# Kernel tuning notes

Hardware: AMD Instinct MI355X
Metric: run time of the kernel (lower is better)

Reference implementation:

```python
import jax, jax.numpy as jnp
import numpy as np

DIM = 1024
NUM_HEADS = 16
HEAD_DIM = DIM // NUM_HEADS  # 64; only used for the softmax scale


def setup_inputs() -> dict:
    key = jax.random.key(0)
    ks = jax.random.split(key, 9)
    s = 1.0 / np.sqrt(DIM)
    return {
        "x": jax.random.normal(ks[0], (2, 4096, DIM), dtype=jnp.float32),
        "Wq": jax.random.normal(ks[1], (DIM, DIM), dtype=jnp.float32) * s,
        "bq": jnp.zeros((DIM,), dtype=jnp.float32),
        "Wk": jax.random.normal(ks[2], (DIM, DIM), dtype=jnp.float32) * s,
        "bk": jnp.zeros((DIM,), dtype=jnp.float32),
        "Wv": jax.random.normal(ks[3], (DIM, DIM), dtype=jnp.float32) * s,
        "bv": jnp.zeros((DIM,), dtype=jnp.float32),
        "Wo": jax.random.normal(ks[4], (DIM, DIM), dtype=jnp.float32) * s,
        "bo": jnp.zeros((DIM,), dtype=jnp.float32),
    }


def reference(x, Wq, bq, Wk, bk, Wv, bv, Wo, bo):
    # Projections (nn.Linear equivalents)
    q = jnp.einsum("bsd,df->bsf", x, Wq) + bq
    k = jnp.einsum("bsd,df->bsf", x, Wk) + bk
    v = jnp.einsum("bsd,df->bsf", x, Wv) + bv
    # Full-dim attention (no head split); scale uses head_dim per original code.
    scale = 1.0 / np.sqrt(HEAD_DIM)
    scores = jnp.einsum("bqd,bkd->bqk", q, k) * scale  # [B, S, S]
    attn = jax.nn.softmax(scores, axis=-1)
    out = jnp.einsum("bqk,bkd->bqd", attn, v)
    return jnp.einsum("bsd,df->bsf", out, Wo) + bo
```

## Files before the change

### kernel.cpp

```cpp
#include <hip/hip_runtime.h>

typedef unsigned short u16;
using bf16x8  = __attribute__((ext_vector_type(8))) __bf16;
using floatx4 = __attribute__((ext_vector_type(4))) float;

__device__ __forceinline__ u16 f2bf(float f) {
  unsigned int u = __builtin_bit_cast(unsigned int, f);
  u += 0x7fffu + ((u >> 16) & 1u);
  return (u16)(u >> 16);
}
__device__ __forceinline__ float bf2f(u16 h) {
  unsigned int u = ((unsigned int)h) << 16;
  return __builtin_bit_cast(float, u);
}

#define AS1(p) ((const __attribute__((address_space(1))) void*)(p))
#define AS3(p) ((__attribute__((address_space(3))) void*)(p))

#define NE_PROLOGUE(bmv, bnv)                                                \
  __shared__ u16 lds[65536];                                    \
  const int tid = threadIdx.x;                                               \
  const int w = tid >> 6, lane = tid & 63;                                   \
  const int wm = (w >> 2) * 128, wn = (w & 3) * 64;                          \
  const int wm16 = (w >> 2) * 8;           \
  const int wn4  = (w & 3) * 4;            \
  const long bm = (bmv), bn = (bnv);                                         \
  floatx4 acc[8][4] = {};                                                    \
  const int fr = lane & 15;                                                  \
  const int kq = (lane >> 4) * 8;                                            \
  const int oc = (lane >> 4) * 4;                                            \
         \
  const int swz  = (lane * 16) ^ (((lane >> 5) & 1) << 5);                   \
  const int srow = swz >> 6;                  \
  const int scol = (swz & 63) >> 1;           \
  const int st0  = w * 2;                      \
                        \
  const int aoff = fr * 64 + ((kq * 2) ^ (((fr >> 3) & 1) << 5));

#define NE_SETUP_PTRS(Abp, Bbp, ldK)                                         \
  const u16* A0p = (Abp) + (long)(st0 * 16 + srow) * (ldK) + scol;           \
  const u16* A1p = A0p + 16L * (ldK);                                        \
  const u16* B0p = (Bbp) + (long)(st0 * 16 + srow) * (ldK) + scol;           \
  const u16* B1p = B0p + 16L * (ldK);

#define NE_SA(T)                                                             \
  { u16* d_ = lds + (((T) & 3) * 16384) + st0 * 512;                         \
    long o_ = (long)(T) * 32;                                                \
    __builtin_amdgcn_global_load_lds(AS1(A0p + o_), AS3(d_), 16, 0, 0);      \
    __builtin_amdgcn_global_load_lds(AS1(A1p + o_), AS3(d_ + 512), 16, 0, 0); }
#define NE_SB(T)                                                             \
  { u16* d_ = lds + (((T) & 3) * 16384) + 8192 + st0 * 512;                  \
    long o_ = (long)(T) * 32;                                                \
    __builtin_amdgcn_global_load_lds(AS1(B0p + o_), AS3(d_), 16, 0, 0);      \
    __builtin_amdgcn_global_load_lds(AS1(B1p + o_), AS3(d_ + 512), 16, 0, 0); }

#define NE_TILE_G(T, NT, MF)                                                 \
  {                                                                          \
    const char* sb_ = (const char*)lds + ((T) & 3) * 32768;                  \
    if ((T) + 2 < (NT)) NE_SB((T) + 2)                                       \
    if ((T) + 3 < (NT)) NE_SA((T) + 3)                                       \
    bf16x8 af[4], bf[4];                                                     \
    _Pragma("unroll")                                                        \
    for (int i = 0; i < 4; ++i)                                              \
      af[i] = *(const bf16x8*)(sb_ + (wm16 + i) * 1024 + aoff);              \
    _Pragma("unroll")                                                        \
    for (int i = 0; i < 4; ++i)                                              \
      bf[i] = *(const bf16x8*)(sb_ + 16384 + (wn4 + i) * 1024 + aoff);       \
    asm volatile("s_waitcnt lgkmcnt(0)" ::: "memory");                       \
    __builtin_amdgcn_sched_barrier(0);                                       \
    __builtin_amdgcn_s_setprio(1);                                           \
    _Pragma("unroll")                                                        \
    for (int mi = 0; mi < 4; ++mi)                                           \
      _Pragma("unroll")                                                      \
      for (int ni = 0; ni < 4; ++ni)                                         \
        acc[mi][ni] = MF(mi, ni, acc[mi][ni]);                               \
    __builtin_amdgcn_s_setprio(0);                                           \
    _Pragma("unroll")                                                        \
    for (int i = 0; i < 4; ++i)                                              \
      af[i] = *(const bf16x8*)(sb_ + (wm16 + 4 + i) * 1024 + aoff);          \
    asm volatile("s_waitcnt lgkmcnt(0)" ::: "memory");                       \
    __builtin_amdgcn_sched_barrier(0);                                       \
    __builtin_amdgcn_s_setprio(1);                                           \
    _Pragma("unroll")                                                        \
    for (int mi = 0; mi < 4; ++mi)                                           \
      _Pragma("unroll")                                                      \
      for (int ni = 0; ni < 4; ++ni)                                         \
        acc[4 + mi][ni] = MF(mi, ni, acc[4 + mi][ni]);                       \
    __builtin_amdgcn_s_setprio(0);                                           \
    if ((T) < (NT) - 3)       { asm volatile("s_waitcnt vmcnt(6)" ::: "memory"); } \
    else if ((T) == (NT) - 3) { asm volatile("s_waitcnt vmcnt(4)" ::: "memory"); } \
    else if ((T) == (NT) - 2) { asm volatile("s_waitcnt vmcnt(0)" ::: "memory"); } \
    __builtin_amdgcn_s_barrier();                                            \
    __builtin_amdgcn_sched_barrier(0);                                       \
  }

#define NE_MF_SWAP(mi, ni, c) __builtin_amdgcn_mfma_f32_16x16x32_bf16(bf[ni], af[mi], (c), 0, 0, 0)
#define NE_MF_NS(mi, ni, c)   __builtin_amdgcn_mfma_f32_16x16x32_bf16(af[mi], bf[ni], (c), 0, 0, 0)
#define NE_TILE(T, NT)    NE_TILE_G(T, NT, NE_MF_SWAP)
#define NE_TILE_NS(T, NT) NE_TILE_G(T, NT, NE_MF_NS)

#define NE_START()                                                           \
  NE_SA(0) NE_SB(0) NE_SA(1) NE_SB(1) NE_SA(2)                               \
  asm volatile("s_waitcnt vmcnt(6)" ::: "memory");                           \
  __builtin_amdgcn_s_barrier();                                              \
  __builtin_amdgcn_sched_barrier(0);

#define NE2_PROLOGUE(bmv, bnv)                                               \
  __shared__ u16 lds[49152];                                     \
  const int tid = threadIdx.x;                                               \
  const int w = tid >> 6, lane = tid & 63;                                   \
  const int wm = (w >> 2) * 64, wn = (w & 3) * 64;                           \
  const int wm4 = (w >> 2) * 4;            \
  const int wn4 = (w & 3) * 4;             \
  const long bm = (bmv), bn = (bnv);                                         \
  floatx4 acc[4][4] = {};                                                    \
  const int fr = lane & 15;                                                  \
  const int kq = (lane >> 4) * 8;                                            \
  const int oc = (lane >> 4) * 4;                                            \
  const int swz  = (lane * 16) ^ (((lane >> 5) & 1) << 5);                   \
  const int srow = swz >> 6;                                                 \
  const int scol = (swz & 63) >> 1;                                          \
  const int st0  = w * 2;                                                    \
  const int aoff = fr * 64 + ((kq * 2) ^ (((fr >> 3) & 1) << 5));

#define NE2_SETUP_PTRS(Abp, Bbp, ldK)                                        \
  const u16* A0p = (Abp) + (long)(w * 16 + srow) * (ldK) + scol;             \
  const u16* B0p = (Bbp) + (long)(st0 * 16 + srow) * (ldK) + scol;           \
  const u16* B1p = B0p + 16L * (ldK);

#define NE2_SA(T)                                                            \
  { u16* d_ = lds + (((T) & 3) * 12288) + w * 512;                           \
    __builtin_amdgcn_global_load_lds(AS1(A0p + (long)(T) * 32), AS3(d_), 16, 0, 0); }
#define NE2_SB(T)                                                            \
  { u16* d_ = lds + (((T) & 3) * 12288) + 4096 + st0 * 512;                  \
    long o_ = (long)(T) * 32;                                                \
    __builtin_amdgcn_global_load_lds(AS1(B0p + o_), AS3(d_), 16, 0, 0);      \
    __builtin_amdgcn_global_load_lds(AS1(B1p + o_), AS3(d_ + 512), 16, 0, 0); }

#define NE2_TILE_G(T, NT, MF)                                                \
  {                                                                          \
    const char* sb_ = (const char*)lds + ((T) & 3) * 24576;                  \
    if ((T) + 2 < (NT)) NE2_SB((T) + 2)                                      \
    if ((T) + 3 < (NT)) NE2_SA((T) + 3)                                      \
    bf16x8 af[4], bf[4];                                                     \
    _Pragma("unroll")                                                        \
    for (int i = 0; i < 4; ++i)                                              \
      af[i] = *(const bf16x8*)(sb_ + (wm4 + i) * 1024 + aoff);               \
    _Pragma("unroll")                                                        \
    for (int i = 0; i < 4; ++i)                                              \
      bf[i] = *(const bf16x8*)(sb_ + 8192 + (wn4 + i) * 1024 + aoff);        \
    asm volatile("s_waitcnt lgkmcnt(0)" ::: "memory");                       \
    __builtin_amdgcn_sched_barrier(0);                                       \
    __builtin_amdgcn_s_setprio(1);                                           \
    _Pragma("unroll")                                                        \
    for (int mi = 0; mi < 4; ++mi)                                           \
      _Pragma("unroll")                                                      \
      for (int ni = 0; ni < 4; ++ni)                                         \
        acc[mi][ni] = MF(mi, ni, acc[mi][ni]);                               \
    __builtin_amdgcn_s_setprio(0);                                           \
    if ((T) < (NT) - 3)       { asm volatile("s_waitcnt vmcnt(4)" ::: "memory"); } \
    else if ((T) == (NT) - 3) { asm volatile("s_waitcnt vmcnt(3)" ::: "memory"); } \
    else if ((T) == (NT) - 2) { asm volatile("s_waitcnt vmcnt(0)" ::: "memory"); } \
    __builtin_amdgcn_s_barrier();                                            \
    __builtin_amdgcn_sched_barrier(0);                                       \
  }

#define NE2_TILE(T, NT)    NE2_TILE_G(T, NT, NE_MF_SWAP)
#define NE2_TILE_NS(T, NT) NE2_TILE_G(T, NT, NE_MF_NS)

#define NE2_START()                                                          \
  NE2_SA(0) NE2_SB(0) NE2_SA(1) NE2_SB(1) NE2_SA(2)                          \
  asm volatile("s_waitcnt vmcnt(4)" ::: "memory");                           \
  __builtin_amdgcn_s_barrier();                                              \
  __builtin_amdgcn_sched_barrier(0);

__global__ __launch_bounds__(512, 2) void gemm_qk_exp(
    const u16* __restrict__ q, const u16* __restrict__ k,
    u16* __restrict__ probs, float* __restrict__ lpartT, float alpha)
{
  const int N = 4096;
  const int xcd = blockIdx.x;
  const int j = blockIdx.y;
  const long b = xcd >> 2;
  const int by = (xcd & 3) * 4 + (j & 3);
  const int bx = j >> 2;

  NE_PROLOGUE((long)by * 256, (long)bx * 256);
  const u16* Ab = q + b * 4096 * 1024 + bm * 1024;
  const u16* Bb = k + b * 4096 * 1024 + bn * 1024;
  NE_SETUP_PTRS(Ab, Bb, 1024);
  u16* P = probs + b * 4096L * 4096;
  float* lp = lpartT + b * 4096 * 64;

  NE_START()
  for (int T = 0; T < 32; ++T) NE_TILE(T, 32)

  const float a2 = alpha * 1.44269504f;
  const int cg = bx * 4 + (w & 3);
#pragma unroll
  for (int mi = 0; mi < 8; ++mi) {
    long row = bm + wm + mi * 16 + fr;
    float rs = 0.f;
#pragma unroll
    for (int ni = 0; ni < 4; ++ni) {
      long colb = bn + wn + ni * 16 + oc;
      float e0 = __builtin_amdgcn_exp2f(acc[mi][ni][0] * a2);
      float e1 = __builtin_amdgcn_exp2f(acc[mi][ni][1] * a2);
      float e2 = __builtin_amdgcn_exp2f(acc[mi][ni][2] * a2);
      float e3 = __builtin_amdgcn_exp2f(acc[mi][ni][3] * a2);
      rs += (e0 + e1) + (e2 + e3);
      ushort4 o;
      o.x = f2bf(e0); o.y = f2bf(e1); o.z = f2bf(e2); o.w = f2bf(e3);
      *(ushort4*)(P + row * N + colb) = o;
    }
    rs += __shfl_xor(rs, 16);
    rs += __shfl_xor(rs, 32);
    if (lane < 16)
      lp[(bm + wm + mi * 16 + lane) * 64 + cg] = rs;
  }
}

__global__ __launch_bounds__(512, 2) void gemm_pv_splitk2(
    const u16* __restrict__ probs, const u16* __restrict__ vT,
    u16* __restrict__ pA, u16* __restrict__ pB)
{
  const int xcd = blockIdx.x;
  const int j = blockIdx.y;
  const long b = xcd >> 2;
  const int sp = (xcd >> 1) & 1;
  const int by = (xcd & 1) * 8 + (j & 7);
  const int bx = j >> 3;

  NE_PROLOGUE((long)by * 256, (long)bx * 256);
  const u16* Ab = probs + b * 4096L * 4096 + bm * 4096 + sp * 2048;
  const u16* Bb = vT + b * 1024L * 4096 + bn * 4096 + sp * 2048;
  NE_SETUP_PTRS(Ab, Bb, 4096);
  u16* part = (b ? pB : pA) + (long)sp * 4096 * 1024;

  NE_START()
  for (int T = 0; T < 64; ++T) NE_TILE(T, 64)

#pragma unroll
  for (int mi = 0; mi < 8; ++mi) {
    long row = bm + wm + mi * 16 + fr;
#pragma unroll
    for (int ni = 0; ni < 4; ++ni) {
      long colb = bn + wn + ni * 16 + oc;
      ushort4 o;
      o.x = f2bf(acc[mi][ni][0]);
      o.y = f2bf(acc[mi][ni][1]);
      o.z = f2bf(acc[mi][ni][2]);
      o.w = f2bf(acc[mi][ni][3]);
      *(ushort4*)(part + row * 1024 + colb) = o;
    }
  }
}

__global__ __launch_bounds__(512, 2) void gemm_qkv(
    const u16* __restrict__ A, const u16* __restrict__ Bt,
    u16* __restrict__ qb, u16* __restrict__ kb, u16* __restrict__ vT,
    const float* __restrict__ bq, const float* __restrict__ bk,
    const float* __restrict__ bv)
{
  const int xcd = blockIdx.x;
  const int j = blockIdx.y;
  const int by = xcd * 8 + (j & 7);
  const int bx = j >> 3;

  NE2_PROLOGUE((long)by * 128, (long)bx * 256);
  const u16* Ab = A + bm * 1024;
  const u16* Bb = Bt + bn * 1024;
  NE2_SETUP_PTRS(Ab, Bb, 1024);

  if (bn < 2048) {
    NE2_START()
    for (int T = 0; T < 32; ++T) NE2_TILE(T, 32)
    u16* C = (bn < 1024) ? qb : kb;
    const float* bias = (bn < 1024) ? bq : bk;
#pragma unroll
    for (int mi = 0; mi < 4; ++mi) {
      long row = bm + wm + mi * 16 + fr;
#pragma unroll
      for (int ni = 0; ni < 4; ++ni) {
        long colg = bn + wn + ni * 16 + oc;
        long cc = colg & 1023;
        float4 bv4 = *(const float4*)(bias + cc);
        ushort4 o;
        o.x = f2bf(acc[mi][ni][0] + bv4.x);
        o.y = f2bf(acc[mi][ni][1] + bv4.y);
        o.z = f2bf(acc[mi][ni][2] + bv4.z);
        o.w = f2bf(acc[mi][ni][3] + bv4.w);
        *(ushort4*)(C + row * 1024 + cc) = o;
      }
    }
  } else {
    NE2_START()
    for (int T = 0; T < 32; ++T) NE2_TILE_NS(T, 32)
    const int orow = (lane >> 4) * 4;
    const long b_ = bm >> 12;
    const long s0 = (bm & 4095) + wm;
    u16* vb = vT + b_ * (1024L * 4096);
#pragma unroll
    for (int ni = 0; ni < 4; ++ni) {
      long d = bn + wn + ni * 16 + fr - 2048;
      float bvv = bv[d];
#pragma unroll
      for (int mi = 0; mi < 4; ++mi) {
        long s = s0 + mi * 16 + orow;
        ushort4 o;
        o.x = f2bf(acc[mi][ni][0] + bvv);
        o.y = f2bf(acc[mi][ni][1] + bvv);
        o.z = f2bf(acc[mi][ni][2] + bvv);
        o.w = f2bf(acc[mi][ni][3] + bvv);
        *(ushort4*)(vb + d * 4096L + s) = o;
      }
    }
  }
}

__global__ __launch_bounds__(512, 2) void gemm_bt(
    const u16* __restrict__ A, const u16* __restrict__ Bt,
    float* __restrict__ Cout, const float* __restrict__ bias)
{
  const int xcd = blockIdx.x;
  const int j = blockIdx.y;
  const int by = xcd * 8 + (j & 7);
  const int bx = j >> 3;

  NE2_PROLOGUE((long)by * 128, (long)bx * 256);
  const u16* Ab = A + bm * 1024;
  const u16* Bb = Bt + bn * 1024;
  NE2_SETUP_PTRS(Ab, Bb, 1024);

  NE2_START()
  for (int T = 0; T < 32; ++T) NE2_TILE(T, 32)

#pragma unroll
  for (int mi = 0; mi < 4; ++mi) {
    long row = bm + wm + mi * 16 + fr;
#pragma unroll
    for (int ni = 0; ni < 4; ++ni) {
      long colb = bn + wn + ni * 16 + oc;
      float4 bv4 = *(const float4*)(bias + colb);
      float4 o;
      o.x = acc[mi][ni][0] + bv4.x;
      o.y = acc[mi][ni][1] + bv4.y;
      o.z = acc[mi][ni][2] + bv4.z;
      o.w = acc[mi][ni][3] + bv4.w;
      *(float4*)(Cout + row * 1024 + colb) = o;
    }
  }
}

__global__ __launch_bounds__(256) void reduce2_div_row(
    const u16* __restrict__ pA, const u16* __restrict__ pB,
    const float* __restrict__ lpartT, u16* __restrict__ ob)
{
  const int row = blockIdx.x;
  const long b = blockIdx.y;
  const int tid = threadIdx.x;
  const u16* part = b ? pB : pA;
  const float* lp = lpartT + b * 4096 * 64;
  __shared__ float sl;
  if (tid < 64) {
    float s = lp[(long)row * 64 + tid];
#pragma unroll
    for (int off = 32; off; off >>= 1) s += __shfl_down(s, off);
    if (tid == 0) sl = s;
  }
  __syncthreads();
  const float inv = 1.0f / sl;
  const long base = (long)row * 1024 + tid * 4;
  float acc4[4] = {0.f, 0.f, 0.f, 0.f};
#pragma unroll
  for (int s = 0; s < 2; ++s) {
    ushort4 p = *(const ushort4*)(part + (long)s * 4096 * 1024 + base);
    acc4[0] += bf2f(p.x); acc4[1] += bf2f(p.y);
    acc4[2] += bf2f(p.z); acc4[3] += bf2f(p.w);
  }
  ushort4 o;
  o.x = f2bf(acc4[0] * inv);
  o.y = f2bf(acc4[1] * inv);
  o.z = f2bf(acc4[2] * inv);
  o.w = f2bf(acc4[3] * inv);
  *(ushort4*)(ob + b * 4096L * 1024 + base) = o;
}

__global__ __launch_bounds__(256) void prep(
    const float* __restrict__ x, u16* __restrict__ xb,
    const float* __restrict__ W0, const float* __restrict__ W1,
    const float* __restrict__ W2, const float* __restrict__ W3,
    u16* __restrict__ O0, u16* __restrict__ O1,
    u16* __restrict__ O2, u16* __restrict__ O3)
{
  __shared__ float tile[32][33];
  int blk = blockIdx.x;
  if (blk < 8192) {
    int i = blk * 256 + threadIdx.x;
    float4 f = ((const float4*)x)[i];
    ushort4 o;
    o.x = f2bf(f.x); o.y = f2bf(f.y); o.z = f2bf(f.z); o.w = f2bf(f.w);
    ((ushort4*)xb)[i] = o;
  } else {
    blk -= 8192;
    const int z = blk >> 10, t = blk & 1023;
    const float* in = (z == 0) ? W0 : (z == 1) ? W1 : (z == 2) ? W2 : W3;
    u16* outp = (z == 0) ? O0 : (z == 1) ? O1 : (z == 2) ? O2 : O3;
    const int bx = (t & 31) * 32, by = (t >> 5) * 32;
    const int tx = threadIdx.x & 31, ty = threadIdx.x >> 5;
    for (int i = ty; i < 32; i += 8)
      tile[i][tx] = in[(long)(by + i) * 1024 + bx + tx];
    __syncthreads();
    for (int i = ty; i < 32; i += 8)
      outp[(long)(bx + i) * 1024 + by + tx] = f2bf(tile[tx][i]);
  }
}

extern "C" void kernel_launch(void* const* d_in, const int* in_sizes, int n_in,
                              void* d_out, int out_size, void* d_ws, size_t ws_size,
                              hipStream_t stream) {
  const float* x  = (const float*)d_in[0];
  const float* Wq = (const float*)d_in[1];
  const float* bq = (const float*)d_in[2];
  const float* Wk = (const float*)d_in[3];
  const float* bk = (const float*)d_in[4];
  const float* Wv = (const float*)d_in[5];
  const float* bv = (const float*)d_in[6];
  const float* Wo = (const float*)d_in[7];
  const float* bo = (const float*)d_in[8];
  float* out = (float*)d_out;

  const int B = 2, S = 4096, D = 1024;
  const long MB = 1L << 20;

  char* w = (char*)d_ws;
  u16* qb  = (u16*)(w);
  u16* kb  = (u16*)(w + 16 * MB);
  u16* vT  = (u16*)(w + 32 * MB);
  u16* xb  = (u16*)(w + 48 * MB);
  u16* ob  = xb;
  u16* WqkvT = (u16*)(w + 64 * MB);
  u16* WoT = WqkvT + 3072L * 1024;
  u16* probs = (u16*)(w + 72 * MB);
  u16* partA = (u16*)(w);
  u16* partB = (u16*)(w + 136 * MB);
  float* lpartT = (float*)d_out;

  prep<<<dim3(8192 + 4096), 256, 0, stream>>>(
      x, xb, Wq, Wk, Wv, Wo,
      WqkvT, WqkvT + 1024L * 1024, WqkvT + 2048L * 1024, WoT);

  gemm_qkv<<<dim3(8, 96), 512, 0, stream>>>(
      xb, WqkvT, qb, kb, vT, bq, bk, bv);

  const float scale = 0.125f;
  gemm_qk_exp<<<dim3(8, 64), 512, 0, stream>>>(
      qb, kb, probs, lpartT, scale);
  gemm_pv_splitk2<<<dim3(8, 32), 512, 0, stream>>>(
      probs, vT, partA, partB);
  reduce2_div_row<<<dim3(S, B), 256, 0, stream>>>(partA, partB, lpartT, ob);

  gemm_bt<<<dim3(8, 32), 512, 0, stream>>>(ob, WoT, out, bo);
}
```

Before: 372.6 us.

## Switch attention GEMMs to 128x256 tiles with 3-stage LDS ring for higher occupancy

Drops the 256x256-tile NE pipeline and moves the QK^T-exp and PV split-K kernels onto the smaller 128x256 NE2 tile, doubling their grid sizes. The NE2 pipeline goes from a 4-slot to a 3-slot LDS ring, with A and B for tile T+2 prefetched together, which cuts shared memory per block. Launch bounds are raised from 2 to 4 blocks per CU to use the lower register and LDS footprint. This trades per-block data reuse and prefetch depth for more resident waves to hide latency.

```diff
diff --git a/kernel.cpp b/kernel.cpp
--- a/kernel.cpp
+++ b/kernel.cpp
@@ -17,96 +17,8 @@
 #define AS1(p) ((const __attribute__((address_space(1))) void*)(p))
 #define AS3(p) ((__attribute__((address_space(3))) void*)(p))
 
-#define NE_PROLOGUE(bmv, bnv)                                                \
-  __shared__ u16 lds[65536];                                    \
-  const int tid = threadIdx.x;                                               \
-  const int w = tid >> 6, lane = tid & 63;                                   \
-  const int wm = (w >> 2) * 128, wn = (w & 3) * 64;                          \
-  const int wm16 = (w >> 2) * 8;           \
-  const int wn4  = (w & 3) * 4;            \
-  const long bm = (bmv), bn = (bnv);                                         \
-  floatx4 acc[8][4] = {};                                                    \
-  const int fr = lane & 15;                                                  \
-  const int kq = (lane >> 4) * 8;                                            \
-  const int oc = (lane >> 4) * 4;                                            \
-         \
-  const int swz  = (lane * 16) ^ (((lane >> 5) & 1) << 5);                   \
-  const int srow = swz >> 6;                  \
-  const int scol = (swz & 63) >> 1;           \
-  const int st0  = w * 2;                      \
-                        \
-  const int aoff = fr * 64 + ((kq * 2) ^ (((fr >> 3) & 1) << 5));
-
-#define NE_SETUP_PTRS(Abp, Bbp, ldK)                                         \
-  const u16* A0p = (Abp) + (long)(st0 * 16 + srow) * (ldK) + scol;           \
-  const u16* A1p = A0p + 16L * (ldK);                                        \
-  const u16* B0p = (Bbp) + (long)(st0 * 16 + srow) * (ldK) + scol;           \
-  const u16* B1p = B0p + 16L * (ldK);
-
-#define NE_SA(T)                                                             \
-  { u16* d_ = lds + (((T) & 3) * 16384) + st0 * 512;                         \
-    long o_ = (long)(T) * 32;                                                \
-    __builtin_amdgcn_global_load_lds(AS1(A0p + o_), AS3(d_), 16, 0, 0);      \
-    __builtin_amdgcn_global_load_lds(AS1(A1p + o_), AS3(d_ + 512), 16, 0, 0); }
-#define NE_SB(T)                                                             \
-  { u16* d_ = lds + (((T) & 3) * 16384) + 8192 + st0 * 512;                  \
-    long o_ = (long)(T) * 32;                                                \
-    __builtin_amdgcn_global_load_lds(AS1(B0p + o_), AS3(d_), 16, 0, 0);      \
-    __builtin_amdgcn_global_load_lds(AS1(B1p + o_), AS3(d_ + 512), 16, 0, 0); }
-
-#define NE_TILE_G(T, NT, MF)                                                 \
-  {                                                                          \
-    const char* sb_ = (const char*)lds + ((T) & 3) * 32768;                  \
-    if ((T) + 2 < (NT)) NE_SB((T) + 2)                                       \
-    if ((T) + 3 < (NT)) NE_SA((T) + 3)                                       \
-    bf16x8 af[4], bf[4];                                                     \
-    _Pragma("unroll")                                                        \
-    for (int i = 0; i < 4; ++i)                                              \
-      af[i] = *(const bf16x8*)(sb_ + (wm16 + i) * 1024 + aoff);              \
-    _Pragma("unroll")                                                        \
-    for (int i = 0; i < 4; ++i)                                              \
-      bf[i] = *(const bf16x8*)(sb_ + 16384 + (wn4 + i) * 1024 + aoff);       \
-    asm volatile("s_waitcnt lgkmcnt(0)" ::: "memory");                       \
-    __builtin_amdgcn_sched_barrier(0);                                       \
-    __builtin_amdgcn_s_setprio(1);                                           \
-    _Pragma("unroll")                                                        \
-    for (int mi = 0; mi < 4; ++mi)                                           \
-      _Pragma("unroll")                                                      \
-      for (int ni = 0; ni < 4; ++ni)                                         \
-        acc[mi][ni] = MF(mi, ni, acc[mi][ni]);                               \
-    __builtin_amdgcn_s_setprio(0);                                           \
-    _Pragma("unroll")                                                        \
-    for (int i = 0; i < 4; ++i)                                              \
-      af[i] = *(const bf16x8*)(sb_ + (wm16 + 4 + i) * 1024 + aoff);          \
-    asm volatile("s_waitcnt lgkmcnt(0)" ::: "memory");                       \
-    __builtin_amdgcn_sched_barrier(0);                                       \
-    __builtin_amdgcn_s_setprio(1);                                           \
-    _Pragma("unroll")                                                        \
-    for (int mi = 0; mi < 4; ++mi)                                           \
-      _Pragma("unroll")                                                      \
-      for (int ni = 0; ni < 4; ++ni)                                         \
-        acc[4 + mi][ni] = MF(mi, ni, acc[4 + mi][ni]);                       \
-    __builtin_amdgcn_s_setprio(0);                                           \
-    if ((T) < (NT) - 3)       { asm volatile("s_waitcnt vmcnt(6)" ::: "memory"); } \
-    else if ((T) == (NT) - 3) { asm volatile("s_waitcnt vmcnt(4)" ::: "memory"); } \
-    else if ((T) == (NT) - 2) { asm volatile("s_waitcnt vmcnt(0)" ::: "memory"); } \
-    __builtin_amdgcn_s_barrier();                                            \
-    __builtin_amdgcn_sched_barrier(0);                                       \
-  }
-
-#define NE_MF_SWAP(mi, ni, c) __builtin_amdgcn_mfma_f32_16x16x32_bf16(bf[ni], af[mi], (c), 0, 0, 0)
-#define NE_MF_NS(mi, ni, c)   __builtin_amdgcn_mfma_f32_16x16x32_bf16(af[mi], bf[ni], (c), 0, 0, 0)
-#define NE_TILE(T, NT)    NE_TILE_G(T, NT, NE_MF_SWAP)
-#define NE_TILE_NS(T, NT) NE_TILE_G(T, NT, NE_MF_NS)
-
-#define NE_START()                                                           \
-  NE_SA(0) NE_SB(0) NE_SA(1) NE_SB(1) NE_SA(2)                               \
-  asm volatile("s_waitcnt vmcnt(6)" ::: "memory");                           \
-  __builtin_amdgcn_s_barrier();                                              \
-  __builtin_amdgcn_sched_barrier(0);
-
 #define NE2_PROLOGUE(bmv, bnv)                                               \
-  __shared__ u16 lds[49152];                                     \
+  __shared__ u16 lds[36864];                          \
   const int tid = threadIdx.x;                                               \
   const int w = tid >> 6, lane = tid & 63;                                   \
   const int wm = (w >> 2) * 64, wn = (w & 3) * 64;                           \
@@ -128,20 +40,22 @@
   const u16* B0p = (Bbp) + (long)(st0 * 16 + srow) * (ldK) + scol;           \
   const u16* B1p = B0p + 16L * (ldK);
 
-#define NE2_SA(T)                                                            \
-  { u16* d_ = lds + (((T) & 3) * 12288) + w * 512;                           \
-    __builtin_amdgcn_global_load_lds(AS1(A0p + (long)(T) * 32), AS3(d_), 16, 0, 0); }
-#define NE2_SB(T)                                                            \
-  { u16* d_ = lds + (((T) & 3) * 12288) + 4096 + st0 * 512;                  \
-    long o_ = (long)(T) * 32;                                                \
+#define NE2_SA(TT, S)                                                        \
+  { u16* d_ = lds + (S) * 12288 + w * 512;                                   \
+    __builtin_amdgcn_global_load_lds(AS1(A0p + (long)(TT) * 32), AS3(d_), 16, 0, 0); }
+#define NE2_SB(TT, S)                                                        \
+  { u16* d_ = lds + (S) * 12288 + 4096 + st0 * 512;                          \
+    long o_ = (long)(TT) * 32;                                               \
     __builtin_amdgcn_global_load_lds(AS1(B0p + o_), AS3(d_), 16, 0, 0);      \
     __builtin_amdgcn_global_load_lds(AS1(B1p + o_), AS3(d_ + 512), 16, 0, 0); }
 
-#define NE2_TILE_G(T, NT, MF)                                                \
+#define NE_MF_SWAP(mi, ni, c) __builtin_amdgcn_mfma_f32_16x16x32_bf16(bf[ni], af[mi], (c), 0, 0, 0)
+#define NE_MF_NS(mi, ni, c)   __builtin_amdgcn_mfma_f32_16x16x32_bf16(af[mi], bf[ni], (c), 0, 0, 0)
+
+#define NE2_TILE_G(T, NT, sR, sW, MF)                                        \
   {                                                                          \
-    const char* sb_ = (const char*)lds + ((T) & 3) * 24576;                  \
-    if ((T) + 2 < (NT)) NE2_SB((T) + 2)                                      \
-    if ((T) + 3 < (NT)) NE2_SA((T) + 3)                                      \
+    const char* sb_ = (const char*)lds + (sR) * 24576;                       \
+    if ((T) + 2 < (NT)) { NE2_SB((T) + 2, sW) NE2_SA((T) + 2, sW) }          \
     bf16x8 af[4], bf[4];                                                     \
     _Pragma("unroll")                                                        \
     for (int i = 0; i < 4; ++i)                                              \
@@ -158,23 +72,32 @@
       for (int ni = 0; ni < 4; ++ni)                                         \
         acc[mi][ni] = MF(mi, ni, acc[mi][ni]);                               \
     __builtin_amdgcn_s_setprio(0);                                           \
-    if ((T) < (NT) - 3)       { asm volatile("s_waitcnt vmcnt(4)" ::: "memory"); } \
-    else if ((T) == (NT) - 3) { asm volatile("s_waitcnt vmcnt(3)" ::: "memory"); } \
+    if ((T) < (NT) - 2)       { asm volatile("s_waitcnt vmcnt(3)" ::: "memory"); } \
     else if ((T) == (NT) - 2) { asm volatile("s_waitcnt vmcnt(0)" ::: "memory"); } \
     __builtin_amdgcn_s_barrier();                                            \
     __builtin_amdgcn_sched_barrier(0);                                       \
   }
 
-#define NE2_TILE(T, NT)    NE2_TILE_G(T, NT, NE_MF_SWAP)
-#define NE2_TILE_NS(T, NT) NE2_TILE_G(T, NT, NE_MF_NS)
-
 #define NE2_START()                                                          \
-  NE2_SA(0) NE2_SB(0) NE2_SA(1) NE2_SB(1) NE2_SA(2)                          \
-  asm volatile("s_waitcnt vmcnt(4)" ::: "memory");                           \
+  NE2_SA(0, 0) NE2_SB(0, 0) NE2_SA(1, 1) NE2_SB(1, 1)                        \
+  asm volatile("s_waitcnt vmcnt(3)" ::: "memory");                           \
   __builtin_amdgcn_s_barrier();                                              \
   __builtin_amdgcn_sched_barrier(0);
 
-__global__ __launch_bounds__(512, 2) void gemm_qk_exp(
+#define NE2_LOOP(NT, TILE_MACRO)                                             \
+  {                                                                          \
+    int sR = 0, sW = 2;                                                      \
+    for (int T = 0; T < (NT); ++T) {                                         \
+      TILE_MACRO(T, (NT), sR, sW)                                            \
+      sR = (sR == 2) ? 0 : sR + 1;                                           \
+      sW = (sW == 2) ? 0 : sW + 1;                                           \
+    }                                                                        \
+  }
+
+#define NE2_TILE(T, NT, sR, sW)    NE2_TILE_G(T, NT, sR, sW, NE_MF_SWAP)
+#define NE2_TILE_NS(T, NT, sR, sW) NE2_TILE_G(T, NT, sR, sW, NE_MF_NS)
+
+__global__ __launch_bounds__(512, 4) void gemm_qk_exp(
     const u16* __restrict__ q, const u16* __restrict__ k,
     u16* __restrict__ probs, float* __restrict__ lpartT, float alpha)
 {
@@ -182,23 +105,23 @@
   const int xcd = blockIdx.x;
   const int j = blockIdx.y;
   const long b = xcd >> 2;
-  const int by = (xcd & 3) * 4 + (j & 3);
-  const int bx = j >> 2;
-
-  NE_PROLOGUE((long)by * 256, (long)bx * 256);
+  const int by = (xcd & 3) * 8 + (j & 7);
+  const int bx = j >> 3;
+
+  NE2_PROLOGUE((long)by * 128, (long)bx * 256);
   const u16* Ab = q + b * 4096 * 1024 + bm * 1024;
   const u16* Bb = k + b * 4096 * 1024 + bn * 1024;
-  NE_SETUP_PTRS(Ab, Bb, 1024);
+  NE2_SETUP_PTRS(Ab, Bb, 1024);
   u16* P = probs + b * 4096L * 4096;
   float* lp = lpartT + b * 4096 * 64;
 
-  NE_START()
-  for (int T = 0; T < 32; ++T) NE_TILE(T, 32)
+  NE2_START()
+  NE2_LOOP(32, NE2_TILE)
 
   const float a2 = alpha * 1.44269504f;
   const int cg = bx * 4 + (w & 3);
 #pragma unroll
-  for (int mi = 0; mi < 8; ++mi) {
+  for (int mi = 0; mi < 4; ++mi) {
     long row = bm + wm + mi * 16 + fr;
     float rs = 0.f;
 #pragma unroll
@@ -220,7 +143,7 @@
   }
 }
 
-__global__ __launch_bounds__(512, 2) void gemm_pv_splitk2(
+__global__ __launch_bounds__(512, 4) void gemm_pv_splitk2(
     const u16* __restrict__ probs, const u16* __restrict__ vT,
     u16* __restrict__ pA, u16* __restrict__ pB)
 {
@@ -228,20 +151,20 @@
   const int j = blockIdx.y;
   const long b = xcd >> 2;
   const int sp = (xcd >> 1) & 1;
-  const int by = (xcd & 1) * 8 + (j & 7);
-  const int bx = j >> 3;
-
-  NE_PROLOGUE((long)by * 256, (long)bx * 256);
+  const int by = (xcd & 1) * 16 + (j & 15);
+  const int bx = j >> 4;
+
+  NE2_PROLOGUE((long)by * 128, (long)bx * 256);
   const u16* Ab = probs + b * 4096L * 4096 + bm * 4096 + sp * 2048;
   const u16* Bb = vT + b * 1024L * 4096 + bn * 4096 + sp * 2048;
-  NE_SETUP_PTRS(Ab, Bb, 4096);
+  NE2_SETUP_PTRS(Ab, Bb, 4096);
   u16* part = (b ? pB : pA) + (long)sp * 4096 * 1024;
 
-  NE_START()
-  for (int T = 0; T < 64; ++T) NE_TILE(T, 64)
-
-#pragma unroll
-  for (int mi = 0; mi < 8; ++mi) {
+  NE2_START()
+  NE2_LOOP(64, NE2_TILE)
+
+#pragma unroll
+  for (int mi = 0; mi < 4; ++mi) {
     long row = bm + wm + mi * 16 + fr;
 #pragma unroll
     for (int ni = 0; ni < 4; ++ni) {
@@ -256,7 +179,7 @@
   }
 }
 
-__global__ __launch_bounds__(512, 2) void gemm_qkv(
+__global__ __launch_bounds__(512, 4) void gemm_qkv(
     const u16* __restrict__ A, const u16* __restrict__ Bt,
     u16* __restrict__ qb, u16* __restrict__ kb, u16* __restrict__ vT,
     const float* __restrict__ bq, const float* __restrict__ bk,
@@ -274,7 +197,7 @@
 
   if (bn < 2048) {
     NE2_START()
-    for (int T = 0; T < 32; ++T) NE2_TILE(T, 32)
+    NE2_LOOP(32, NE2_TILE)
     u16* C = (bn < 1024) ? qb : kb;
     const float* bias = (bn < 1024) ? bq : bk;
 #pragma unroll
@@ -295,7 +218,7 @@
     }
   } else {
     NE2_START()
-    for (int T = 0; T < 32; ++T) NE2_TILE_NS(T, 32)
+    NE2_LOOP(32, NE2_TILE_NS)
     const int orow = (lane >> 4) * 4;
     const long b_ = bm >> 12;
     const long s0 = (bm & 4095) + wm;
@@ -318,7 +241,7 @@
   }
 }
 
-__global__ __launch_bounds__(512, 2) void gemm_bt(
+__global__ __launch_bounds__(512, 4) void gemm_bt(
     const u16* __restrict__ A, const u16* __restrict__ Bt,
     float* __restrict__ Cout, const float* __restrict__ bias)
 {
@@ -333,7 +256,7 @@
   NE2_SETUP_PTRS(Ab, Bb, 1024);
 
   NE2_START()
-  for (int T = 0; T < 32; ++T) NE2_TILE(T, 32)
+  NE2_LOOP(32, NE2_TILE)
 
 #pragma unroll
   for (int mi = 0; mi < 4; ++mi) {
@@ -454,9 +377,9 @@
       xb, WqkvT, qb, kb, vT, bq, bk, bv);
 
   const float scale = 0.125f;
-  gemm_qk_exp<<<dim3(8, 64), 512, 0, stream>>>(
+  gemm_qk_exp<<<dim3(8, 128), 512, 0, stream>>>(
       qb, kb, probs, lpartT, scale);
-  gemm_pv_splitk2<<<dim3(8, 32), 512, 0, stream>>>(
+  gemm_pv_splitk2<<<dim3(8, 64), 512, 0, stream>>>(
       probs, vT, partA, partB);
   reduce2_div_row<<<dim3(S, B), 256, 0, stream>>>(partA, partB, lpartT, ob);
 
```

After: 363.2 us. 2.5% less time.
